# Kernel tuning notes

Hardware: AMD Instinct MI355X
Metric: run time of the kernel (lower is better)

The kernel has to match this reference:

```python
import jax, jax.numpy as jnp
import numpy as np

N = 50000      # nodes
E = 800000     # edges (avg degree 16)
NF = 128       # input feature dim
H = 128        # hidden dim
GAMMA = 1.0    # gm init arg
COS_EPS = 1e-8 # F.cosine_similarity eps
EW_MIN = 1e-4  # edge-weight clamp


def setup_inputs() -> dict:
    key = jax.random.key(0)
    ks = jax.random.split(key, 9)
    x = jax.random.normal(ks[0], (N, NF), dtype=jnp.float32)
    edge_index = jax.random.randint(ks[1], (2, E), 0, N, dtype=jnp.int64)
    sensitive_attr = jax.random.randint(ks[2], (N,), 0, 2, dtype=jnp.int64)
    s1 = 1.0 / np.sqrt(NF)
    s2 = 1.0 / np.sqrt(H)
    W1 = jax.random.normal(ks[3], (NF, H), dtype=jnp.float32) * s1
    b1 = jnp.zeros((H,), dtype=jnp.float32)
    W2 = jax.random.normal(ks[4], (H, H), dtype=jnp.float32) * s2
    b2 = jnp.zeros((H,), dtype=jnp.float32)
    Wc = jax.random.normal(ks[5], (H, 1), dtype=jnp.float32) * s2
    bc = jnp.zeros((1,), dtype=jnp.float32)
    return {"x": x, "edge_index": edge_index, "sensitive_attr": sensitive_attr,
            "W1": W1, "b1": b1, "W2": W2, "b2": b2, "Wc": Wc, "bc": bc}


def gcn_conv(x, W, b, src, dst, ew, n):
    """PyG GCNConv: lin -> symmetric-normalized edge-weighted aggregation (+self loops) -> bias."""
    xt = x @ W                                              # [N,H]
    deg = jax.ops.segment_sum(ew, dst, num_segments=n) + 1.0  # self-loop weight 1
    dinv = jnp.where(deg > 0, deg ** -0.5, 0.0)             # [N]
    norm = dinv[src] * ew * dinv[dst]                       # [E]
    agg = jax.ops.segment_sum(xt[src] * norm[:, None], dst, num_segments=n)
    # self-loop contribution: norm_ii = dinv[i] * 1 * dinv[i]
    return agg + xt * (dinv * dinv)[:, None] + b


def reference(x, edge_index, sensitive_attr, W1, b1, W2, b2, Wc, bc):
    src, dst = edge_index[0], edge_index[1]
    # cosine-similarity edge weights (gather-heavy)
    xs, xd = x[src], x[dst]                                  # [E,F] each
    dot = jnp.sum(xs * xd, axis=1)
    ns = jnp.maximum(jnp.sqrt(jnp.sum(xs * xs, axis=1)), COS_EPS)
    nd = jnp.maximum(jnp.sqrt(jnp.sum(xd * xd, axis=1)), COS_EPS)
    sim = dot / (ns * nd)
    sen_diff = (sensitive_attr[src] != sensitive_attr[dst]).astype(x.dtype)
    ew = jnp.maximum(sim * jnp.exp(-GAMMA * sen_diff), EW_MIN)
    # two GCN layers (dropout is identity in eval mode)
    h = jax.nn.relu(gcn_conv(x, W1, b1, src, dst, ew, N))
    h = jax.nn.relu(gcn_conv(h, W2, b2, src, dst, ew, N))
    y = h @ Wc + bc                                          # [N,1]
    return (y, h)
```

## Files before the change

kernel.cpp:

```cpp
#include <hip/hip_runtime.h>


typedef unsigned short u16;
typedef unsigned int u32;
typedef __attribute__((ext_vector_type(8))) short short8;
typedef __attribute__((ext_vector_type(4))) float floatx4;

__device__ __forceinline__ float bflo(u32 u){ return __uint_as_float(u << 16); }
__device__ __forceinline__ float bfhi(u32 u){ return __uint_as_float(u & 0xFFFF0000u); }
__device__ __forceinline__ float bf1(u16 u){ return __uint_as_float(((u32)u) << 16); }
__device__ __forceinline__ u16 f2bf(float f){
    u32 u = __float_as_uint(f);
    u += 0x7FFFu + ((u >> 16) & 1u);
    return (u16)(u >> 16);
}
__device__ __forceinline__ u32 pack2(float a, float b){
    return (u32)f2bf(a) | ((u32)f2bf(b) << 16);
}
__device__ __forceinline__ float wsum(float v){
#pragma unroll
    for (int o = 32; o > 0; o >>= 1) v += __shfl_xor(v, o, 64);
    return v;
}
__device__ __forceinline__ float ld1(const void* p, size_t idx, int f32){
    return f32 ? ((const float*)p)[idx] : bf1(((const u16*)p)[idx]);
}
__device__ __forceinline__ int ldidx(const int* p, size_t i, int i64){
    return i64 ? p[2 * i] : p[i];
}

__global__ void classify_k(const u32* __restrict__ xw, const int* __restrict__ eiw,
                           int* __restrict__ flags, int* __restrict__ bcnt)
{
    __shared__ int c_out, c_nz;
    int t = threadIdx.x;
    if (t == 0) { c_out = 0; c_nz = 0; }
    if (t < 256) bcnt[t] = 0;
    __syncthreads();
    u32 w = xw[t];
    int e = (w >> 7) & 0xFF;
    int outl = (e < 110 || e > 140) ? 1 : 0;
    int nz = (eiw[2 * t + 1] != 0) ? 1 : 0;
    atomicAdd(&c_out, outl);
    atomicAdd(&c_nz, nz);
    __syncthreads();
    if (t == 0) { flags[0] = (c_out > 256); flags[1] = (c_nz < 256); }
}

__global__ __launch_bounds__(256) void convhist_k(const void* __restrict__ x,
                                                  u32* __restrict__ xb,
                                                  float* __restrict__ rn, int N,
                                                  const int* __restrict__ ei,
                                                  const int* __restrict__ sa,
                                                  int* __restrict__ bcnt, int E,
                                                  const void* __restrict__ W1,
                                                  const void* __restrict__ W2,
                                                  uint4* __restrict__ wf1,
                                                  uint4* __restrict__ wf2,
                                                  const int* __restrict__ flags,
                                                  int nbN, int nbH)
{
    __shared__ int lb[256];
    int b = blockIdx.x;
    if (b < nbN) {
        int i = b * 4 + (threadIdx.x >> 6);
        if (i >= N) return;
        int lane = threadIdx.x & 63;
        u32 u;
        if (flags[0]) {
            const float* q = (const float*)x + (size_t)i * 128 + lane * 2;
            u = pack2(q[0], q[1]);
        } else u = ((const u32*)x)[(size_t)i * 64 + lane];
        xb[(size_t)i * 64 + lane] = u;
        float f0 = bflo(u), f1 = bfhi(u);
        float ss = wsum(f0 * f0 + f1 * f1);
        if (lane == 0) {
            float r = 1.0f / fmaxf(sqrtf(ss), 1e-8f);
            int a = flags[1] ? sa[2 * (size_t)i] : sa[i];
            rn[i] = a ? -r : r;
        }
    } else if (b < nbN + nbH) {
        int t = threadIdx.x;
        lb[t] = 0;
        __syncthreads();
        int i64 = flags[1];
        size_t base = (size_t)(b - nbN) * 8192;
#pragma unroll 4
        for (int k = 0; k < 32; ++k) {
            size_t e = base + (size_t)k * 256 + t;
            if (e < (size_t)E) {
                int d = ldidx(ei, (size_t)E + e, i64);
                if ((u32)d >= (u32)N) d = 0;
                atomicAdd(&lb[d >> 8], 1);
            }
        }
        __syncthreads();
        int c = lb[t];
        if (c) atomicAdd(&bcnt[t], c);
    } else {
        int slot = (b - nbN - nbH) * 256 + threadIdx.x;
        if (slot >= 4096) return;
        int f32w = flags[0];
        const void* W = (slot < 2048) ? W1 : W2;
        uint4* wf = (slot < 2048) ? wf1 : wf2;
        int s = slot & 2047;
        int lane = s & 63, kk = (s >> 6) & 3, ct = s >> 8;
        int q = lane >> 4, n = lane & 15;
        int col = ct * 16 + n, k0 = kk * 32 + q * 8;
        union { u16 us[8]; uint4 u4; } tmp;
#pragma unroll
        for (int j = 0; j < 8; ++j)
            tmp.us[j] = f2bf(ld1(W, (size_t)(k0 + j) * 128 + col, f32w));
        wf[s] = tmp.u4;
    }
}

__global__ void bscan_k(const int* __restrict__ bcnt, int* __restrict__ bbase,
                        int* __restrict__ bcur, int* __restrict__ rowp, int N)
{
    int lane = threadIdx.x;
    int carry = 0;
    for (int base = 0; base < 256; base += 64) {
        int i = base + lane;
        int v = bcnt[i];
        int sc = v;
#pragma unroll
        for (int o = 1; o < 64; o <<= 1) {
            int nv = __shfl_up(sc, o);
            if (lane >= o) sc += nv;
        }
        int excl = carry + sc - v;
        bbase[i] = excl;
        bcur[i] = excl;
        carry += __shfl(sc, 63);
    }
    if (lane == 0) { bbase[256] = carry; rowp[N] = carry; }
}

__global__ __launch_bounds__(256) void bucket_k(const int* __restrict__ ei,
                                                int* __restrict__ bcur,
                                                u32* __restrict__ tmp,
                                                int E, int N,
                                                const int* __restrict__ flags)
{
    __shared__ int lh[256];
    __shared__ int gb[256];
    int t = threadIdx.x;
    lh[t] = 0;
    __syncthreads();
    int i64 = flags[1];
    size_t base = (size_t)blockIdx.x * 4096;
    u32 pay[16], meta[16];
#pragma unroll
    for (int k = 0; k < 16; ++k) {
        size_t e = base + (size_t)k * 256 + t;
        if (e < (size_t)E) {
            int s = ldidx(ei, e, i64);
            int d = ldidx(ei, (size_t)E + e, i64);
            if ((u32)s >= (u32)N) s = 0;
            if ((u32)d >= (u32)N) d = 0;
            int b = d >> 8;
            pay[k] = ((u32)s << 8) | ((u32)d & 0xFFu);
            int r = atomicAdd(&lh[b], 1);
            meta[k] = ((u32)r << 8) | (u32)b;
        } else meta[k] = 0xFFFFFFFFu;
    }
    __syncthreads();
    int c = lh[t];
    gb[t] = c ? atomicAdd(&bcur[t], c) : 0;
    __syncthreads();
#pragma unroll
    for (int k = 0; k < 16; ++k) {
        if (meta[k] != 0xFFFFFFFFu) {
            int b = (int)(meta[k] & 0xFFu);
            int r = (int)(meta[k] >> 8);
            tmp[gb[b] + r] = pay[k];
        }
    }
}

__global__ __launch_bounds__(256) void scat2_k(const int* __restrict__ bbase,
                                               int* __restrict__ rowp,
                                               const u32* __restrict__ tmp,
                                               u32* __restrict__ rec,
                                               int N, int E)
{
    __shared__ int lcnt[256];
    __shared__ int wtot[4];
    int b = blockIdx.x, t = threadIdx.x;
    int lane = t & 63, w = t >> 6;
    int n0 = b << 8;
    int p0 = bbase[b], p1 = bbase[b + 1];
    if (p0 < 0) p0 = 0;
    if (p1 > E) p1 = E;
    lcnt[t] = 0;
    __syncthreads();
    for (int idx = p0 + t; idx < p1; idx += 256)
        atomicAdd(&lcnt[tmp[idx] & 0xFFu], 1);
    __syncthreads();
    int v = lcnt[t];
    int sc = v;
#pragma unroll
    for (int o = 1; o < 64; o <<= 1) {
        int nv = __shfl_up(sc, o);
        if (lane >= o) sc += nv;
    }
    if (lane == 63) wtot[w] = sc;
    __syncthreads();
    int wo = 0;
#pragma unroll
    for (int k = 0; k < 4; ++k) { int s = wtot[k]; if (k < w) wo += s; }
    int excl = wo + sc - v;
    int node = n0 + t;
    if (node < N) rowp[node] = p0 + excl;
    lcnt[t] = excl;
    __syncthreads();
    for (int idx = p0 + t; idx < p1; idx += 256) {
        u32 pay = tmp[idx];
        int r = atomicAdd(&lcnt[pay & 0xFFu], 1);
        int pos = p0 + r;
        if ((u32)pos >= (u32)E) pos = 0;
        rec[pos] = pay >> 8;
    }
}

__global__ __launch_bounds__(256) void ewcsr_k(const u32* __restrict__ xb,
                                               const float* __restrict__ rn,
                                               const int* __restrict__ rowp,
                                               u32* __restrict__ rec,
                                               float* __restrict__ dv,
                                               int N, int E)
{
    int i = blockIdx.x * 4 + (threadIdx.x >> 6);
    if (i >= N) return;
    int lane = threadIdx.x & 63, g = lane >> 4, j = lane & 15;
    uint4 D = ((const uint4*)(xb + (size_t)i * 64))[j];
    float rni = rn[i];
    int p0 = rowp[i], p1 = rowp[i + 1];
    if (p0 < 0) p0 = 0;
    if (p1 > E) p1 = E;
    float acc = 0.0f;
    int p = p0 + g;
    for (; p + 4 < p1; p += 8) {
        int s0 = (int)rec[p];     if ((u32)s0 >= (u32)N) s0 = 0;
        int s1 = (int)rec[p + 4]; if ((u32)s1 >= (u32)N) s1 = 0;
        uint4 A0 = ((const uint4*)(xb + (size_t)s0 * 64))[j];
        uint4 A1 = ((const uint4*)(xb + (size_t)s1 * 64))[j];
        float d0 = bflo(A0.x) * bflo(D.x) + bfhi(A0.x) * bfhi(D.x)
                 + bflo(A0.y) * bflo(D.y) + bfhi(A0.y) * bfhi(D.y)
                 + bflo(A0.z) * bflo(D.z) + bfhi(A0.z) * bfhi(D.z)
                 + bflo(A0.w) * bflo(D.w) + bfhi(A0.w) * bfhi(D.w);
        float d1 = bflo(A1.x) * bflo(D.x) + bfhi(A1.x) * bfhi(D.x)
                 + bflo(A1.y) * bflo(D.y) + bfhi(A1.y) * bfhi(D.y)
                 + bflo(A1.z) * bflo(D.z) + bfhi(A1.z) * bfhi(D.z)
                 + bflo(A1.w) * bflo(D.w) + bfhi(A1.w) * bfhi(D.w);
#pragma unroll
        for (int o = 8; o > 0; o >>= 1) {
            d0 += __shfl_xor(d0, o);
            d1 += __shfl_xor(d1, o);
        }
        if (j == 0) {
            float pr0 = rn[s0] * rni;
            float w0 = fmaxf(d0 * fabsf(pr0) *
                             ((pr0 < 0.0f) ? 0.36787944117144233f : 1.0f), 1e-4f);
            u16 wb0 = f2bf(w0);
            rec[p] = ((u32)s0 << 16) | wb0;
            acc += bf1(wb0);
            float pr1 = rn[s1] * rni;
            float w1 = fmaxf(d1 * fabsf(pr1) *
                             ((pr1 < 0.0f) ? 0.36787944117144233f : 1.0f), 1e-4f);
            u16 wb1 = f2bf(w1);
            rec[p + 4] = ((u32)s1 << 16) | wb1;
            acc += bf1(wb1);
        }
    }
    if (p < p1) {
        int s0 = (int)rec[p]; if ((u32)s0 >= (u32)N) s0 = 0;
        uint4 A0 = ((const uint4*)(xb + (size_t)s0 * 64))[j];
        float d0 = bflo(A0.x) * bflo(D.x) + bfhi(A0.x) * bfhi(D.x)
                 + bflo(A0.y) * bflo(D.y) + bfhi(A0.y) * bfhi(D.y)
                 + bflo(A0.z) * bflo(D.z) + bfhi(A0.z) * bfhi(D.z)
                 + bflo(A0.w) * bflo(D.w) + bfhi(A0.w) * bfhi(D.w);
#pragma unroll
        for (int o = 8; o > 0; o >>= 1) d0 += __shfl_xor(d0, o);
        if (j == 0) {
            float pr0 = rn[s0] * rni;
            float w0 = fmaxf(d0 * fabsf(pr0) *
                             ((pr0 < 0.0f) ? 0.36787944117144233f : 1.0f), 1e-4f);
            u16 wb0 = f2bf(w0);
            rec[p] = ((u32)s0 << 16) | wb0;
            acc += bf1(wb0);
        }
    }
    acc += __shfl_xor(acc, 16);
    acc += __shfl_xor(acc, 32);
    if (lane == 0) dv[i] = 1.0f / sqrtf(1.0f + acc);
}

__global__ __launch_bounds__(256) void aggemm_k(const u32* __restrict__ feat,
                                                const int* __restrict__ rowp,
                                                const u32* __restrict__ rec,
                                                const float* __restrict__ dinv,
                                                const uint4* __restrict__ wfrag,
                                                const void* __restrict__ bias,
                                                void* __restrict__ out, int outbf,
                                                int N, int E,
                                                const void* __restrict__ Wc,
                                                const void* __restrict__ bc,
                                                float* __restrict__ yout,
                                                const int* __restrict__ flags)
{
    __shared__ u32 T[64 * 68];
    int t = threadIdx.x, wave = t >> 6, lane = t & 63;
    int rowbase = blockIdx.x * 64 + wave * 16;
    for (int r = 0; r < 16; ++r) {
        int i = rowbase + r;
        float a0 = 0.0f, a1 = 0.0f;
        if (i < N) {
            float di = dinv[i], sc = di * di;
            u32 u = feat[(size_t)i * 64 + lane];
            a0 = bflo(u) * sc; a1 = bfhi(u) * sc;
            int p0 = rowp[i], p1 = rowp[i + 1];
            if (p0 < 0) p0 = 0;
            if (p1 > E) p1 = E;
            int p = p0;
            for (; p + 7 < p1; p += 8) {
                u32 rr[8]; int s[8]; u32 v[8];
#pragma unroll
                for (int k = 0; k < 8; ++k) {
                    rr[k] = rec[p + k];
                    s[k] = rr[k] >> 16;
                    if (s[k] >= N) s[k] = 0;
                }
#pragma unroll
                for (int k = 0; k < 8; ++k) v[k] = feat[(size_t)s[k] * 64 + lane];
#pragma unroll
                for (int k = 0; k < 8; ++k) {
                    float w = bf1((u16)rr[k]) * di * dinv[s[k]];
                    a0 = fmaf(w, bflo(v[k]), a0);
                    a1 = fmaf(w, bfhi(v[k]), a1);
                }
            }
            for (; p + 1 < p1; p += 2) {
                u32 r0 = rec[p], r1 = rec[p + 1];
                int s0 = r0 >> 16, s1 = r1 >> 16;
                if (s0 >= N) s0 = 0;
                if (s1 >= N) s1 = 0;
                u32 v0 = feat[(size_t)s0 * 64 + lane];
                u32 v1 = feat[(size_t)s1 * 64 + lane];
                float w0 = bf1((u16)r0) * di * dinv[s0];
                float w1 = bf1((u16)r1) * di * dinv[s1];
                a0 = fmaf(w0, bflo(v0), a0); a1 = fmaf(w0, bfhi(v0), a1);
                a0 = fmaf(w1, bflo(v1), a0); a1 = fmaf(w1, bfhi(v1), a1);
            }
            if (p < p1) {
                u32 r0 = rec[p];
                int s0 = r0 >> 16;
                if (s0 >= N) s0 = 0;
                u32 v0 = feat[(size_t)s0 * 64 + lane];
                float w0 = bf1((u16)r0) * di * dinv[s0];
                a0 = fmaf(w0, bflo(v0), a0); a1 = fmaf(w0, bfhi(v0), a1);
            }
        }
        T[(wave * 16 + r) * 68 + lane] = pack2(a0, a1);
    }
    __syncthreads();
    int q = lane >> 4, n = lane & 15;
    int f32w = flags[0];
    const u32* ap = T + (size_t)(wave * 16 + n) * 68;
    short8 a[4];
#pragma unroll
    for (int kk = 0; kk < 4; ++kk) {
        uint4 av = *(const uint4*)(ap + (kk * 4 + q) * 4);
        a[kk] = *(short8*)&av;
    }
    floatx4 acc[8];
#pragma unroll
    for (int ct = 0; ct < 8; ++ct) acc[ct] = (floatx4){0.f, 0.f, 0.f, 0.f};
#pragma unroll
    for (int ct = 0; ct < 8; ++ct) {
#pragma unroll
        for (int kk = 0; kk < 4; ++kk) {
            uint4 bv = wfrag[(ct * 4 + kk) * 64 + lane];
            acc[ct] = __builtin_amdgcn_mfma_f32_16x16x32_bf16(
                a[kk], *(short8*)&bv, acc[ct], 0, 0, 0);
        }
    }
    float bcv = 0.0f;
    float part[4] = {0.f, 0.f, 0.f, 0.f};
    if (yout) bcv = ld1(bc, 0, f32w);
#pragma unroll
    for (int ct = 0; ct < 8; ++ct) {
        int col = ct * 16 + n;
        float bia = ld1(bias, col, f32w);
        float wcv = yout ? ld1(Wc, col, f32w) : 0.0f;
#pragma unroll
        for (int r = 0; r < 4; ++r) {
            int row = rowbase + q * 4 + r;
            float h = fmaxf(acc[ct][r] + bia, 0.0f);
            if (row < N) {
                if (outbf) ((u16*)out)[(size_t)row * 128 + col] = f2bf(h);
                else       ((float*)out)[(size_t)row * 128 + col] = h;
            }
            part[r] = fmaf(h, wcv, part[r]);
        }
    }
    if (yout) {
#pragma unroll
        for (int r = 0; r < 4; ++r) {
            float pr = part[r];
#pragma unroll
            for (int o = 8; o > 0; o >>= 1) pr += __shfl_xor(pr, o);
            int row = rowbase + q * 4 + r;
            if (n == 0 && row < N) yout[row] = pr + bcv;
        }
    }
}

extern "C" void kernel_launch(void* const* d_in, const int* in_sizes, int n_in,
                              void* d_out, int out_size, void* d_ws, size_t ws_size,
                              hipStream_t stream)
{
    const void* x  = d_in[0];
    const int* ei  = (const int*)d_in[1];
    const int* sa  = (const int*)d_in[2];
    const void* W1 = d_in[3];
    const void* b1 = d_in[4];
    const void* W2 = d_in[5];
    const void* b2 = d_in[6];
    const void* Wc = d_in[7];
    const void* bc = d_in[8];
    const int N = in_sizes[2];
    const int E = in_sizes[1] / 2;

    float* y_out = (float*)d_out;
    float* h_out = y_out + N;
    u32*   h1b   = (u32*)d_in[0];
    u32*   tmp   = (u32*)d_in[0];

    const int nbN = (N + 3) / 4;
    const int nbH = (E + 8191) / 8192;
    const int NB  = (N + 255) / 256;

    char* p = (char*)d_ws;
    auto carve = [&](size_t bytes) { char* r = p; p += (bytes + 255) & ~(size_t)255; return r; };
    int*   flags = (int*)carve(256);
    float* rn    = (float*)carve((size_t)N * 4);
    float* dinv  = (float*)carve((size_t)N * 4);
    int*   rowp  = (int*)carve((size_t)(N + 1) * 4);
    int*   bcnt  = (int*)carve(256 * 4);
    int*   bbase = (int*)carve(260 * 4);
    int*   bcur  = (int*)carve(256 * 4);
    uint4* wf1   = (uint4*)carve(2048 * 16);
    uint4* wf2   = (uint4*)carve(2048 * 16);
    u32*   rec   = (u32*)carve((size_t)E * 4);
    u32*   xb    = (u32*)carve((size_t)N * 64 * 4);

    classify_k<<<1, 1024, 0, stream>>>((const u32*)x, ei, flags, bcnt);
    convhist_k<<<nbN + nbH + 16, 256, 0, stream>>>(x, xb, rn, N, ei, sa, bcnt, E,
                                                   W1, W2, wf1, wf2, flags,
                                                   nbN, nbH);
    bscan_k<<<1, 64, 0, stream>>>(bcnt, bbase, bcur, rowp, N);
    bucket_k<<<(E + 4095) / 4096, 256, 0, stream>>>(ei, bcur, tmp, E, N, flags);
    scat2_k<<<NB, 256, 0, stream>>>(bbase, rowp, tmp, rec, N, E);
    ewcsr_k<<<(N + 3) / 4, 256, 0, stream>>>(xb, rn, rowp, rec, dinv, N, E);

    aggemm_k<<<(N + 63) / 64, 256, 0, stream>>>(xb, rowp, rec, dinv, wf1, b1,
                                                h1b, 1, N, E,
                                                nullptr, nullptr, nullptr, flags);
    aggemm_k<<<(N + 63) / 64, 256, 0, stream>>>(h1b, rowp, rec, dinv, wf2, b2,
                                                h_out, 0, N, E,
                                                Wc, bc, y_out, flags);
}
```

Before: 318.2 us.

## Stream edges across a wave's 16 rows as one flat segmented loop

Instead of processing each destination row's edge list separately with per-row tail loops, each wave walks the contiguous CSR edge range for its 16 rows in batches of 16 edges. Segment boundaries are detected with row pointers and dinv values held in registers and read via shuffles, and partial sums are flushed into an fp32 LDS accumulator seeded with the self-loop term. This is meant to keep more gathers in flight and cut tail-loop overhead for low-degree rows, at the cost of more registers, a larger fp32 LDS tile, and divergent flush branches.

```diff
diff --git a/kernel.cpp b/kernel.cpp
--- a/kernel.cpp
+++ b/kernel.cpp
@@ -310,68 +310,131 @@
                                                 float* __restrict__ yout,
                                                 const int* __restrict__ flags)
 {
-    __shared__ u32 T[64 * 68];
+    __shared__ float Acc[4][16][132];
     int t = threadIdx.x, wave = t >> 6, lane = t & 63;
     int rowbase = blockIdx.x * 64 + wave * 16;
+
+    int idx = rowbase + lane;
+    int rbreg = E;
+    if (lane < 17) {
+        int ii = idx < N ? idx : N;
+        int v = rowp[ii];
+        rbreg = v < 0 ? 0 : (v > E ? E : v);
+    }
+    float dreg = 0.0f;
+    if (lane < 16 && idx < N) dreg = dinv[idx];
+
     for (int r = 0; r < 16; ++r) {
         int i = rowbase + r;
-        float a0 = 0.0f, a1 = 0.0f;
+        float s0 = 0.0f, s1 = 0.0f;
         if (i < N) {
-            float di = dinv[i], sc = di * di;
+            float di = __shfl(dreg, r), sc = di * di;
             u32 u = feat[(size_t)i * 64 + lane];
-            a0 = bflo(u) * sc; a1 = bfhi(u) * sc;
-            int p0 = rowp[i], p1 = rowp[i + 1];
-            if (p0 < 0) p0 = 0;
-            if (p1 > E) p1 = E;
-            int p = p0;
-            for (; p + 7 < p1; p += 8) {
-                u32 rr[8]; int s[8]; u32 v[8];
-#pragma unroll
-                for (int k = 0; k < 8; ++k) {
-                    rr[k] = rec[p + k];
-                    s[k] = rr[k] >> 16;
-                    if (s[k] >= N) s[k] = 0;
-                }
-#pragma unroll
-                for (int k = 0; k < 8; ++k) v[k] = feat[(size_t)s[k] * 64 + lane];
-#pragma unroll
-                for (int k = 0; k < 8; ++k) {
-                    float w = bf1((u16)rr[k]) * di * dinv[s[k]];
-                    a0 = fmaf(w, bflo(v[k]), a0);
-                    a1 = fmaf(w, bfhi(v[k]), a1);
-                }
+            s0 = bflo(u) * sc; s1 = bfhi(u) * sc;
+        }
+        float2 st; st.x = s0; st.y = s1;
+        *(float2*)&Acc[wave][r][2 * lane] = st;
+    }
+
+    int P0 = __shfl(rbreg, 0), P16 = __shfl(rbreg, 16);
+    int crow = 0;
+    int nb = __shfl(rbreg, 1);
+    float dic = __shfl(dreg, 0);
+    float a0 = 0.0f, a1 = 0.0f;
+    int p = P0;
+    for (; p + 15 < P16; p += 16) {
+        u32 rr[16]; int s[16]; u32 v[16]; float dvs[16];
+#pragma unroll
+        for (int k = 0; k < 16; ++k) {
+            rr[k] = rec[p + k];
+            s[k] = rr[k] >> 16;
+            if (s[k] >= N) s[k] = 0;
+        }
+#pragma unroll
+        for (int k = 0; k < 16; ++k) v[k] = feat[(size_t)s[k] * 64 + lane];
+#pragma unroll
+        for (int k = 0; k < 16; ++k) dvs[k] = dinv[s[k]];
+#pragma unroll
+        for (int k = 0; k < 16; ++k) {
+            int e = p + k;
+            if (e >= nb) {
+                float2* ap = (float2*)&Acc[wave][crow][2 * lane];
+                float2 cv = *ap; cv.x += a0; cv.y += a1; *ap = cv;
+                do { ++crow; nb = __shfl(rbreg, crow + 1); } while (e >= nb);
+                dic = __shfl(dreg, crow & 15);
+                a0 = 0.0f; a1 = 0.0f;
             }
-            for (; p + 1 < p1; p += 2) {
-                u32 r0 = rec[p], r1 = rec[p + 1];
-                int s0 = r0 >> 16, s1 = r1 >> 16;
-                if (s0 >= N) s0 = 0;
-                if (s1 >= N) s1 = 0;
-                u32 v0 = feat[(size_t)s0 * 64 + lane];
-                u32 v1 = feat[(size_t)s1 * 64 + lane];
-                float w0 = bf1((u16)r0) * di * dinv[s0];
-                float w1 = bf1((u16)r1) * di * dinv[s1];
-                a0 = fmaf(w0, bflo(v0), a0); a1 = fmaf(w0, bfhi(v0), a1);
-                a0 = fmaf(w1, bflo(v1), a0); a1 = fmaf(w1, bfhi(v1), a1);
+            float w = bf1((u16)rr[k]) * dic * dvs[k];
+            a0 = fmaf(w, bflo(v[k]), a0);
+            a1 = fmaf(w, bfhi(v[k]), a1);
+        }
+    }
+    for (; p + 3 < P16; p += 4) {
+        u32 rr[4]; int s[4]; u32 v[4]; float dvs[4];
+#pragma unroll
+        for (int k = 0; k < 4; ++k) {
+            rr[k] = rec[p + k];
+            s[k] = rr[k] >> 16;
+            if (s[k] >= N) s[k] = 0;
+        }
+#pragma unroll
+        for (int k = 0; k < 4; ++k) v[k] = feat[(size_t)s[k] * 64 + lane];
+#pragma unroll
+        for (int k = 0; k < 4; ++k) dvs[k] = dinv[s[k]];
+#pragma unroll
+        for (int k = 0; k < 4; ++k) {
+            int e = p + k;
+            if (e >= nb) {
+                float2* ap = (float2*)&Acc[wave][crow][2 * lane];
+                float2 cv = *ap; cv.x += a0; cv.y += a1; *ap = cv;
+                do { ++crow; nb = __shfl(rbreg, crow + 1); } while (e >= nb);
+                dic = __shfl(dreg, crow & 15);
+                a0 = 0.0f; a1 = 0.0f;
             }
-            if (p < p1) {
-                u32 r0 = rec[p];
-                int s0 = r0 >> 16;
-                if (s0 >= N) s0 = 0;
-                u32 v0 = feat[(size_t)s0 * 64 + lane];
-                float w0 = bf1((u16)r0) * di * dinv[s0];
-                a0 = fmaf(w0, bflo(v0), a0); a1 = fmaf(w0, bfhi(v0), a1);
-            }
-        }
-        T[(wave * 16 + r) * 68 + lane] = pack2(a0, a1);
-    }
-    __syncthreads();
+            float w = bf1((u16)rr[k]) * dic * dvs[k];
+            a0 = fmaf(w, bflo(v[k]), a0);
+            a1 = fmaf(w, bfhi(v[k]), a1);
+        }
+    }
+    for (; p < P16; ++p) {
+        u32 r0 = rec[p];
+        int s0 = r0 >> 16;
+        if (s0 >= N) s0 = 0;
+        u32 v0 = feat[(size_t)s0 * 64 + lane];
+        float dv0 = dinv[s0];
+        if (p >= nb) {
+            float2* ap = (float2*)&Acc[wave][crow][2 * lane];
+            float2 cv = *ap; cv.x += a0; cv.y += a1; *ap = cv;
+            do { ++crow; nb = __shfl(rbreg, crow + 1); } while (p >= nb);
+            dic = __shfl(dreg, crow & 15);
+            a0 = 0.0f; a1 = 0.0f;
+        }
+        float w = bf1((u16)r0) * dic * dv0;
+        a0 = fmaf(w, bflo(v0), a0);
+        a1 = fmaf(w, bfhi(v0), a1);
+    }
+    {
+        float2* ap = (float2*)&Acc[wave][crow & 15][2 * lane];
+        float2 cv = *ap; cv.x += a0; cv.y += a1; *ap = cv;
+    }
+    __syncthreads();
+
     int q = lane >> 4, n = lane & 15;
     int f32w = flags[0];
-    const u32* ap = T + (size_t)(wave * 16 + n) * 68;
+    const float* rowptr = &Acc[wave][n][0];
     short8 a[4];
 #pragma unroll
     for (int kk = 0; kk < 4; ++kk) {
-        uint4 av = *(const uint4*)(ap + (kk * 4 + q) * 4);
+        int c0 = kk * 32 + q * 8;
+        float2 g0 = *(const float2*)(rowptr + c0);
+        float2 g1 = *(const float2*)(rowptr + c0 + 2);
+        float2 g2 = *(const float2*)(rowptr + c0 + 4);
+        float2 g3 = *(const float2*)(rowptr + c0 + 6);
+        uint4 av;
+        av.x = pack2(g0.x, g0.y);
+        av.y = pack2(g1.x, g1.y);
+        av.z = pack2(g2.x, g2.y);
+        av.w = pack2(g3.x, g3.y);
         a[kk] = *(short8*)&av;
     }
     floatx4 acc[8];
@@ -396,7 +459,8 @@
         float wcv = yout ? ld1(Wc, col, f32w) : 0.0f;
 #pragma unroll
         for (int r = 0; r < 4; ++r) {
-            int row = rowbase + q * 4 + r;
+            int row = rowbase - wave * 16 + wave * 16 + q * 4 + r;
+            row = blockIdx.x * 64 + wave * 16 + q * 4 + r;
             float h = fmaxf(acc[ct][r] + bia, 0.0f);
             if (row < N) {
                 if (outbf) ((u16*)out)[(size_t)row * 128 + col] = f2bf(h);
@@ -411,7 +475,7 @@
             float pr = part[r];
 #pragma unroll
             for (int o = 8; o > 0; o >>= 1) pr += __shfl_xor(pr, o);
-            int row = rowbase + q * 4 + r;
+            int row = blockIdx.x * 64 + wave * 16 + q * 4 + r;
             if (n == 0 && row < N) yout[row] = pr + bcv;
         }
     }
```

Result: faster. 285.6 us (-10.2%).
